# Kernel optimization log

Hardware: AMD Instinct MI355X
Metric: run time of the kernel (lower is better)

Reference implementation:

```python
import jax, jax.numpy as jnp
import numpy as np

N, P, F, E = 4096, 512, 4096, 65536
FN, FE = 32, 32
H, C = 4, 64
D = H * C
HL = 64
LMAX, LFMAX = 256, 16


def _bn(x, g, b):
    m = x.mean(0)
    v = jnp.mean((x - m) ** 2, 0)
    return (x - m) / jnp.sqrt(v + 1e-5) * g + b


def _gat(x, src, dst, eattr, W, We, asrc, adst, aedge, bias):
    # PyG GATConv with edge_dim: self-loops appended with fill_value='mean' edge attrs
    n = x.shape[0]
    cnt = jax.ops.segment_sum(jnp.ones((eattr.shape[0],), eattr.dtype), dst, n)
    sums = jax.ops.segment_sum(eattr, dst, n)
    loop_attr = jnp.where(cnt[:, None] > 0, sums / jnp.maximum(cnt, 1.0)[:, None], 0.0)
    loops = jnp.arange(n, dtype=src.dtype)
    s2 = jnp.concatenate([src, loops])
    d2 = jnp.concatenate([dst, loops])
    ea = jnp.concatenate([eattr, loop_attr], 0)
    h = (x @ W).reshape(n, H, C)
    e = (ea @ We).reshape(-1, H, C)
    logits = jax.nn.leaky_relu((h * asrc).sum(-1)[s2] + (h * adst).sum(-1)[d2] + (e * aedge).sum(-1), 0.2)
    mx = jax.ops.segment_max(logits, d2, n)
    w = jnp.exp(logits - mx[d2])
    alpha = w / jax.ops.segment_sum(w, d2, n)[d2]  # softmax over incoming edges per dst
    out = jax.ops.segment_sum(h[s2] * alpha[:, :, None], d2, n).reshape(n, D) + bias
    return out, s2, d2, alpha


def _lstm(seq, Wih, Whh, bih, bhh):
    # torch single-layer batch_first LSTM; gate order i,f,g,o
    B = seq.shape[0]
    hid = Whh.shape[1]
    def step(carry, xt):
        hp, cp = carry
        z = xt @ Wih.T + hp @ Whh.T + bih + bhh
        i, f, g, o = jnp.split(z, 4, axis=-1)
        c = jax.nn.sigmoid(f) * cp + jax.nn.sigmoid(i) * jnp.tanh(g)
        hh = jax.nn.sigmoid(o) * jnp.tanh(c)
        return (hh, c), hh
    init = (jnp.zeros((B, hid), seq.dtype), jnp.zeros((B, hid), seq.dtype))
    _, ys = jax.lax.scan(step, init, seq.transpose(1, 0, 2))
    return ys.transpose(1, 0, 2)


def _pack(x, mask_f, max_len):
    # scatter node ids into [S, max_len] slots (cumsum positions), then gather x
    mask = mask_f > 0.5
    n, S = mask.shape
    lengths = mask.sum(0)
    pos = jnp.cumsum(mask, 0) - 1
    slot = jnp.where(mask, jnp.arange(S)[None, :] * max_len + pos, S * max_len)
    node_ids = jnp.broadcast_to(jnp.arange(n, dtype=jnp.int32)[:, None], (n, S))
    buf = jnp.zeros(S * max_len + 1, jnp.int32).at[slot.reshape(-1)].set(node_ids.reshape(-1))
    nfs = buf[: S * max_len].reshape(S, max_len)
    valid = jnp.arange(max_len)[None, :] < lengths[:, None]
    seq = jnp.where(valid[:, :, None], x[nfs], 0.0)
    return seq, lengths


def _node_seq(x, mask_f, max_len, Wih, Whh, bih, bhh):
    seq, lengths = _pack(x, mask_f, max_len)
    out = _lstm(seq, Wih, Whh, bih, bhh)
    return out[jnp.arange(seq.shape[0]), lengths - 1]


def _splice(x, src_f, snk_f, emap, alpha, max_len, Wih, Whh, bih, bhh):
    # pair k-th source True with k-th sink True in row-major flatten order (torch masked-select semantics)
    src_m = src_f > 0.5
    snk_m = snk_f > 0.5
    n, S = src_m.shape
    lengths = src_m.sum(0)
    pos = jnp.cumsum(src_m, 0) - 1
    node_ids = jnp.broadcast_to(jnp.arange(n, dtype=jnp.int32)[:, None], (n, S)).reshape(-1)
    srcf = src_m.reshape(-1)
    snkf = snk_m.reshape(-1)
    total = n * S
    rank_snk = jnp.cumsum(snkf) - 1
    snk_by_rank = jnp.zeros(total + 1, jnp.int32).at[jnp.where(snkf, rank_snk, total)].set(node_ids)
    paired = snk_by_rank[jnp.cumsum(srcf) - 1]
    slot = jnp.where(src_m, jnp.arange(S)[None, :] * max_len + pos, S * max_len).reshape(-1)
    sbuf = jnp.zeros(S * max_len + 1, jnp.int32).at[slot].set(node_ids)
    tbuf = jnp.zeros(S * max_len + 1, jnp.int32).at[slot].set(paired)
    sn = sbuf[: S * max_len].reshape(S, max_len)
    tn = tbuf[: S * max_len].reshape(S, max_len)
    att = alpha[emap[sn * n + tn]]  # [S, T, H]
    se = (x[sn].reshape(S, max_len, H, C) * att[..., None]).reshape(S, max_len, D)
    te = (x[tn].reshape(S, max_len, H, C) * att[..., None]).reshape(S, max_len, D)
    emb = jnp.concatenate([se, te], -1)
    valid = jnp.arange(max_len)[None, :] < lengths[:, None]
    emb = jnp.where(valid[:, :, None], emb, 0.0)
    out = _lstm(emb, Wih, Whh, bih, bhh)
    return out[jnp.arange(S), lengths - 1]


def _compat(paths, frags):
    # mismatch-count reformulation of ((path==frag) | ~span_mask).all(0): exact for 0/1 masks
    n = paths.shape[0]
    relevance = (paths.T @ frags) > 0.0
    fb = frags > 0.5
    fs = jnp.argmax(fb, 0)
    fe = n - 1 - jnp.argmax(fb[::-1], 0)
    r = jnp.arange(n)[:, None]
    fmask = ((r >= fs[None, :]) & (r <= fe[None, :])).astype(paths.dtype)
    mism = frags.T @ (1.0 - paths) + (fmask - frags).T @ paths  # [F, P]
    compat = mism.T == 0.0
    pos = (relevance & compat).astype(paths.dtype)
    neg = (relevance & (~compat)).astype(paths.dtype)
    return pos, neg


def reference(x, edge_index, edge_attr, candidate_paths, candidate_paths_source, candidate_paths_sink, path_abundance, fragments, bn_x_g, bn_x_b, bn_e_g, bn_e_b, gat0_W, gat0_We, gat0_asrc, gat0_adst, gat0_aedge, gat0_bias, gat1_W, gat1_We, gat1_asrc, gat1_adst, gat1_aedge, gat1_bias, node_Wih, node_Whh, node_bih, node_bhh, splice_Wih, splice_Whh, splice_bih, splice_bhh, frag_Wih, frag_Whh, frag_bih, frag_bhh, fc1_W, fc1_b, fc2_W, fc2_b):
    xn = _bn(x, bn_x_g, bn_x_b)
    ea = _bn(edge_attr, bn_e_g, bn_e_b)
    src, dst = edge_index[0], edge_index[1]
    h, _, _, _ = _gat(xn, src, dst, ea, gat0_W, gat0_We, gat0_asrc, gat0_adst, gat0_aedge, gat0_bias)
    h = jax.nn.elu(h)
    h, s2, d2, alpha = _gat(h, src, dst, ea, gat1_W, gat1_We, gat1_asrc, gat1_adst, gat1_aedge, gat1_bias)
    h = jax.nn.elu(h)
    n = h.shape[0]
    emap = jnp.zeros(n * n, jnp.int32).at[s2 * n + d2].set(jnp.arange(s2.shape[0], dtype=jnp.int32))
    node_emb = _node_seq(h, candidate_paths, LMAX, node_Wih, node_Whh, node_bih, node_bhh)
    splice_emb = _splice(h, candidate_paths_source, candidate_paths_sink, emap, alpha, LMAX, splice_Wih, splice_Whh, splice_bih, splice_bhh)
    path_emb = jnp.concatenate([node_emb, splice_emb, path_abundance[:, None]], -1)
    frag_emb = _node_seq(h, fragments, LFMAX, frag_Wih, frag_Whh, frag_bih, frag_bhh)
    pos, neg = _compat(candidate_paths, fragments)
    combined = jnp.concatenate([path_emb, pos @ frag_emb, neg @ frag_emb], -1)
    score = jax.nn.relu(combined @ fc1_W.T + fc1_b) @ fc2_W.T + fc2_b
    return jax.nn.sigmoid(score[:, 0])


def setup_inputs():
    rng = np.random.default_rng(0)
    keys = jax.random.split(jax.random.key(0), 40)
    idx = np.arange(N)[:, None]
    ps = rng.integers(0, N - LMAX, P)
    pl = rng.integers(16, LMAX + 1, P)
    cp = ((idx >= ps) & (idx < ps + pl)).astype(np.float32)
    cps = ((idx >= ps) & (idx < ps + pl - 1)).astype(np.float32)
    cpk = ((idx >= ps + 1) & (idx < ps + pl)).astype(np.float32)
    fst = rng.integers(0, N - LFMAX, F)
    fl = rng.integers(2, LFMAX + 1, F)
    fr = ((idx >= fst) & (idx < fst + fl)).astype(np.float32)
    # unique off-diagonal edges; first N-1 are consecutive (n, n+1) so splice lookups hit real edges
    consec = np.arange(N - 1) * (N - 1) + np.arange(N - 1)
    r_rand = rng.choice(N * (N - 1), size=E, replace=False)
    r = np.concatenate([consec, np.setdiff1d(r_rand, consec)])[:E]
    esrc = r // (N - 1)
    rem = r % (N - 1)
    edst = rem + (rem >= esrc)
    edge_index = jnp.asarray(np.stack([esrc, edst]).astype(np.int32))
    g = lambda k, s, sc=0.1: jax.random.normal(keys[k], s, jnp.float32) * sc
    return dict(
        x=g(0, (N, FN), 1.0),
        edge_index=edge_index,
        edge_attr=g(1, (E, FE), 1.0),
        candidate_paths=jnp.asarray(cp),
        candidate_paths_source=jnp.asarray(cps),
        candidate_paths_sink=jnp.asarray(cpk),
        path_abundance=jax.random.uniform(keys[2], (P,)),
        fragments=jnp.asarray(fr),
        bn_x_g=jnp.ones((FN,)), bn_x_b=jnp.zeros((FN,)),
        bn_e_g=jnp.ones((FE,)), bn_e_b=jnp.zeros((FE,)),
        gat0_W=g(3, (FN, D)), gat0_We=g(4, (FE, D)), gat0_asrc=g(5, (H, C)), gat0_adst=g(6, (H, C)), gat0_aedge=g(7, (H, C)), gat0_bias=g(8, (D,)),
        gat1_W=g(9, (D, D)), gat1_We=g(10, (FE, D)), gat1_asrc=g(11, (H, C)), gat1_adst=g(12, (H, C)), gat1_aedge=g(13, (H, C)), gat1_bias=g(14, (D,)),
        node_Wih=g(15, (4 * HL, D)), node_Whh=g(16, (4 * HL, HL)), node_bih=g(17, (4 * HL,)), node_bhh=g(18, (4 * HL,)),
        splice_Wih=g(19, (4 * HL, 2 * D)), splice_Whh=g(20, (4 * HL, HL)), splice_bih=g(21, (4 * HL,)), splice_bhh=g(22, (4 * HL,)),
        frag_Wih=g(23, (4 * HL, D)), frag_Whh=g(24, (4 * HL, HL)), frag_bih=g(25, (4 * HL,)), frag_bhh=g(26, (4 * HL,)),
        fc1_W=g(27, (HL, 4 * HL + 1)), fc1_b=g(28, (HL,)), fc2_W=g(29, (1, HL)), fc2_b=g(30, (1,)),
    )
```

## Files before the change

### kernel.cpp

```cpp
#include <hip/hip_runtime.h>


constexpr int cN = 4096, cP = 512, cE = 65536, cF = 4096, cM = cE + cN;
constexpr int cLMAX = 256;

typedef float f32x4 __attribute__((ext_vector_type(4)));

#define DEV __device__ __forceinline__
DEV float sigf(float x)  { return 1.f / (1.f + __expf(-x)); }
DEV float tanhx(float x) { return 2.f / (1.f + __expf(-2.f * x)) - 1.f; }
DEV float eluf(float x)  { return x > 0.f ? x : (__expf(x) - 1.f); }
DEV float lrelu(float x) { return x > 0.f ? x : 0.2f * x; }

#define LBAR() asm volatile("s_waitcnt lgkmcnt(0)\n\ts_barrier" ::: "memory")

__global__ void init_k(float* bnst, int* deg, int* cursor,
                       int* p_s, int* p_e, int* s_s, int* s_e,
                       int* f_s, int* f_e) {
  int i = blockIdx.x * 256 + threadIdx.x;
  if (i < 128) bnst[i] = 0.f;
  if (i < cN) { deg[i] = 0; cursor[i] = 0; f_s[i] = 0x7fffffff; f_e[i] = -1; }
  if (i < cP) { p_s[i] = 0x7fffffff; p_e[i] = -1; s_s[i] = 0x7fffffff; s_e[i] = -1; }
}

__global__ void bn_stats(const float* __restrict__ x, int rows,
                         float* sums, float* sumsq) {
  int tid = threadIdx.x;
  long total = (long)rows * 32;
  float s = 0.f, q = 0.f;
  for (long i = (long)blockIdx.x * 256 + tid; i < total; i += (long)gridDim.x * 256) {
    float v = x[i]; s += v; q += v * v;
  }
  __shared__ float ls[256], lq[256];
  ls[tid] = s; lq[tid] = q; __syncthreads();
  if (tid < 32) {
    float S = 0.f, Q = 0.f;
    for (int j = tid; j < 256; j += 32) { S += ls[j]; Q += lq[j]; }
    atomicAdd(&sums[tid], S); atomicAdd(&sumsq[tid], Q);
  }
}

__global__ void prep_small(const float* bnst,
    const float* xg, const float* xb, const float* eg, const float* eb,
    const float* We0, const float* ae0, const float* We1, const float* ae1,
    const float* nbih, const float* nbhh, const float* fbih, const float* fbhh,
    const float* sbih, const float* sbhh,
    float* scaleX, float* shiftX, float* scaleE, float* shiftE,
    float* q0, float* q1, float* nb, float* fb, float* sbb) {
  int tid = threadIdx.x;
  if (tid < 32) {
    float m = bnst[tid] / (float)cN;
    float v = bnst[32 + tid] / (float)cN - m * m;
    float sc = xg[tid] * rsqrtf(v + 1e-5f);
    scaleX[tid] = sc; shiftX[tid] = xb[tid] - m * sc;
  } else if (tid < 64) {
    int c = tid - 32;
    float m = bnst[64 + c] / (float)cE;
    float v = bnst[96 + c] / (float)cE - m * m;
    float sc = eg[c] * rsqrtf(v + 1e-5f);
    scaleE[c] = sc; shiftE[c] = eb[c] - m * sc;
  }
  if (tid < 128) {
    int k = tid >> 2, hh = tid & 3;
    float s0 = 0.f, s1 = 0.f;
    for (int c = 0; c < 64; c++) {
      s0 += We0[k * 256 + hh * 64 + c] * ae0[hh * 64 + c];
      s1 += We1[k * 256 + hh * 64 + c] * ae1[hh * 64 + c];
    }
    q0[tid] = s0; q1[tid] = s1;
  }
  nb[tid] = nbih[tid] + nbhh[tid];
  fb[tid] = fbih[tid] + fbhh[tid];
  sbb[tid] = sbih[tid] + sbhh[tid];
}

__global__ void bn_apply(const float* __restrict__ x, const float* __restrict__ e,
                         const float* scX, const float* shX,
                         const float* scE, const float* shE,
                         float* xn, float* ea) {
  long t1 = (long)cN * 32, t2 = t1 + (long)cE * 32;
  for (long i = (long)blockIdx.x * 256 + threadIdx.x; i < t2; i += (long)gridDim.x * 256) {
    if (i < t1) { int c = (int)(i & 31); xn[i] = x[i] * scX[c] + shX[c]; }
    else { long j = i - t1; int c = (int)(j & 31); ea[j] = e[j] * scE[c] + shE[c]; }
  }
}

__global__ void deg_count(const int* __restrict__ ei, int* deg) {
  int m = blockIdx.x * 256 + threadIdx.x;
  if (m < cE) atomicAdd(&deg[ei[cE + m]], 1);
}

__global__ void scan_offsets(const int* __restrict__ deg, int* offs) {
  __shared__ int tsum[256]; __shared__ int tpre[257];
  int tid = threadIdx.x;
  int base = tid * 16, s = 0; int loc[16];
  for (int i = 0; i < 16; i++) { loc[i] = s; s += deg[base + i] + 1; }
  tsum[tid] = s; __syncthreads();
  if (tid == 0) { int r = 0; for (int j = 0; j < 256; j++) { tpre[j] = r; r += tsum[j]; } tpre[256] = r; }
  __syncthreads();
  for (int i = 0; i < 16; i++) offs[base + i] = tpre[tid] + loc[i];
  if (tid == 255) offs[cN] = tpre[256];
}

__global__ void csr_fill(const int* __restrict__ ei, const int* __restrict__ offs,
                         int* cursor, int* eids) {
  int m = blockIdx.x * 256 + threadIdx.x;
  if (m < cE) {
    int d = ei[cE + m];
    int pos = atomicAdd(&cursor[d], 1);
    eids[offs[d] + pos] = m;
  } else if (m < cM) {
    int n = m - cE;
    int pos = atomicAdd(&cursor[n], 1);
    eids[offs[n] + pos] = m;
  }
}

__global__ void loop_attr_k(const float* __restrict__ ea, const int* __restrict__ offs,
                            const int* __restrict__ eids,
                            const float* q0, const float* q1,
                            float* es0, float* es1) {
  int n = blockIdx.x, tid = threadIdx.x;
  __shared__ float la[32];
  int o0 = offs[n], o1 = offs[n + 1];
  if (tid < 32) {
    float s = 0.f; int cnt = 0;
    for (int x = o0; x < o1; x++) {
      int eid = eids[x];
      if (eid < cE) { s += ea[(size_t)eid * 32 + tid]; cnt++; }
    }
    la[tid] = cnt > 0 ? s / (float)cnt : 0.f;
  }
  __syncthreads();
  if (tid < 8) {
    int hh = tid & 3;
    const float* q = (tid < 4) ? q0 : q1;
    float s = 0.f;
    for (int k = 0; k < 32; k++) s += la[k] * q[k * 4 + hh];
    ((tid < 4) ? es0 : es1)[(size_t)(cE + n) * 4 + hh] = s;
  }
}

template <bool NT, bool PERM>
__global__ __launch_bounds__(256) void gemm(const float* __restrict__ A,
                                            const float* __restrict__ B,
                                            const float* __restrict__ bias,
                                            float* __restrict__ C,
                                            int M, int Nc, int K,
                                            int lda, int ldb, int ldc) {
  __shared__ float As[16][65];
  __shared__ float Bs[16][68];
  int nb = Nc / 64;
  int bx = blockIdx.x % nb, by = blockIdx.x / nb;
  int j0 = bx * 64, i0 = by * 64;
  int tid = threadIdx.x, tx = tid % 16, ty = tid / 16;
  float acc[4][4] = {};
  for (int k0 = 0; k0 < K; k0 += 16) {
    for (int l = tid; l < 1024; l += 256) {
      int r = l >> 4, c = l & 15;
      As[c][r] = A[(size_t)(i0 + r) * lda + k0 + c];
    }
    if (NT) {
      for (int l = tid; l < 1024; l += 256) {
        int r = l >> 4, c = l & 15;
        Bs[c][r] = B[(size_t)(j0 + r) * ldb + k0 + c];
      }
    } else {
      for (int l = tid; l < 1024; l += 256) {
        int j = l & 63, c = l >> 6;
        Bs[c][j] = B[(size_t)(k0 + c) * ldb + j0 + j];
      }
    }
    __syncthreads();
#pragma unroll
    for (int kk = 0; kk < 16; kk++) {
      float av[4], bv[4];
#pragma unroll
      for (int u = 0; u < 4; u++) { av[u] = As[kk][ty * 4 + u]; bv[u] = Bs[kk][tx * 4 + u]; }
#pragma unroll
      for (int u = 0; u < 4; u++)
#pragma unroll
        for (int v = 0; v < 4; v++) acc[u][v] = fmaf(av[u], bv[v], acc[u][v]);
    }
    __syncthreads();
  }
#pragma unroll
  for (int u = 0; u < 4; u++)
#pragma unroll
    for (int v = 0; v < 4; v++) {
      int i = i0 + ty * 4 + u, j = j0 + tx * 4 + v;
      float r = acc[u][v] + (bias ? bias[j] : 0.f);
      int jj = PERM ? (((j & 63) << 2) | (j >> 6)) : j;
      C[(size_t)i * ldc + jj] = r;
    }
}

__global__ __launch_bounds__(256) void gemm_g(const float* __restrict__ hf,
                                              const float* __restrict__ sWih,
                                              float* __restrict__ Gp) {
  int bid = blockIdx.x;
  int hh = bid & 3, jt = (bid >> 2) & 3, mt = bid >> 4;
  int i0 = mt * 64, j0 = jt * 64;
  __shared__ float As[16][65];
  __shared__ float Bs[16][68];
  int tid = threadIdx.x, tx = tid & 15, ty = tid >> 4;
  float acc[4][4] = {};
  for (int k0 = 0; k0 < 128; k0 += 16) {
    int second = (k0 >= 64);
    int kb = hh * 64 + (k0 & 63);
    for (int l = tid; l < 1024; l += 256) {
      int r = l >> 4, c = l & 15;
      int row = i0 + r + second;
      As[c][r] = (row < cN) ? hf[(size_t)row * 256 + kb + c] : 0.f;
    }
    for (int l = tid; l < 1024; l += 256) {
      int r = l >> 4, c = l & 15;
      Bs[c][r] = sWih[(size_t)(j0 + r) * 512 + second * 256 + kb + c];
    }
    __syncthreads();
#pragma unroll
    for (int kk = 0; kk < 16; kk++) {
      float av[4], bv[4];
#pragma unroll
      for (int u = 0; u < 4; u++) { av[u] = As[kk][ty * 4 + u]; bv[u] = Bs[kk][tx * 4 + u]; }
#pragma unroll
      for (int u = 0; u < 4; u++)
#pragma unroll
        for (int v = 0; v < 4; v++) acc[u][v] = fmaf(av[u], bv[v], acc[u][v]);
    }
    __syncthreads();
  }
#pragma unroll
  for (int u = 0; u < 4; u++)
#pragma unroll
    for (int v = 0; v < 4; v++) {
      int i = i0 + ty * 4 + u, j = j0 + tx * 4 + v;
      int g = j >> 6, un = j & 63;
      Gp[(size_t)i * 1024 + un * 16 + g * 4 + hh] = acc[u][v];
    }
}

__global__ void node_scores(const float* __restrict__ h, const float* __restrict__ asrc,
                            const float* __restrict__ adst, float* ssrc, float* sdst) {
  int idx = blockIdx.x * 256 + threadIdx.x;
  if (idx >= cN * 4) return;
  int n = idx >> 2, hh = idx & 3;
  float s1 = 0.f, s2 = 0.f;
  const float* hr = h + (size_t)n * 256 + hh * 64;
  const float* a1 = asrc + hh * 64;
  const float* a2 = adst + hh * 64;
  for (int c = 0; c < 64; c++) { float v = hr[c]; s1 += v * a1[c]; s2 += v * a2[c]; }
  ssrc[idx] = s1; sdst[idx] = s2;
}

__global__ void es_edges(const float* __restrict__ ea, const float* __restrict__ q,
                         float* es) {
  int m = blockIdx.x * 256 + threadIdx.x;
  if (m >= cE) return;
  float a0 = 0.f, a1 = 0.f, a2 = 0.f, a3 = 0.f;
  const float4* r4 = (const float4*)(ea + (size_t)m * 32);
#pragma unroll
  for (int k4 = 0; k4 < 8; k4++) {
    float4 v = r4[k4];
    int k = k4 * 4;
    a0 += v.x * q[k * 4] + v.y * q[(k + 1) * 4] + v.z * q[(k + 2) * 4] + v.w * q[(k + 3) * 4];
    a1 += v.x * q[k * 4 + 1] + v.y * q[(k + 1) * 4 + 1] + v.z * q[(k + 2) * 4 + 1] + v.w * q[(k + 3) * 4 + 1];
    a2 += v.x * q[k * 4 + 2] + v.y * q[(k + 1) * 4 + 2] + v.z * q[(k + 2) * 4 + 2] + v.w * q[(k + 3) * 4 + 2];
    a3 += v.x * q[k * 4 + 3] + v.y * q[(k + 1) * 4 + 3] + v.z * q[(k + 2) * 4 + 3] + v.w * q[(k + 3) * 4 + 3];
  }
  float* o = es + (size_t)m * 4;
  o[0] = a0; o[1] = a1; o[2] = a2; o[3] = a3;
}

__global__ __launch_bounds__(256) void gat_agg(
    const float* __restrict__ hfeat, const float* __restrict__ ssrc,
    const float* __restrict__ sdst, const float* __restrict__ es,
    const int* __restrict__ offs, const int* __restrict__ eids,
    const int* __restrict__ ei, const float* __restrict__ bias,
    float* __restrict__ out, float* alpha_out) {
  int n = blockIdx.x, tid = threadIdx.x;
  __shared__ float l_lds[1024 * 4];
  __shared__ int s_lds[1024];
  __shared__ float red[4];
  int o0 = offs[n], o1 = offs[n + 1];
  int deg = o1 - o0; if (deg > 1024) deg = 1024;
  for (int idx = tid; idx < deg * 4; idx += 256) {
    int e = idx >> 2, hh = idx & 3;
    int eid = eids[o0 + e];
    int src = (eid < cE) ? ei[eid] : n;
    if (hh == 0) s_lds[e] = src;
    float lg = ssrc[src * 4 + hh] + sdst[n * 4 + hh] + es[(size_t)eid * 4 + hh];
    l_lds[idx] = lrelu(lg);
  }
  __syncthreads();
  if (tid < 4) {
    float mx = -1e30f;
    for (int e = 0; e < deg; e++) mx = fmaxf(mx, l_lds[e * 4 + tid]);
    float sm = 0.f;
    for (int e = 0; e < deg; e++) {
      float w = __expf(l_lds[e * 4 + tid] - mx);
      l_lds[e * 4 + tid] = w; sm += w;
    }
    red[tid] = 1.f / sm;
  }
  __syncthreads();
  for (int idx = tid; idx < deg * 4; idx += 256) {
    int e = idx >> 2, hh = idx & 3;
    float a = l_lds[idx] * red[hh];
    l_lds[idx] = a;
    if (alpha_out) { int eid = eids[o0 + e]; alpha_out[(size_t)eid * 4 + hh] = a; }
  }
  __syncthreads();
  int c = tid, hh = c >> 6;
  float acc = 0.f;
  for (int e = 0; e < deg; e++)
    acc = fmaf(l_lds[e * 4 + hh], hfeat[(size_t)s_lds[e] * 256 + c], acc);
  acc += bias[c];
  out[(size_t)n * 256 + c] = eluf(acc);
}

__global__ void intervals_k(const float* __restrict__ cp, const float* __restrict__ cps,
                            const float* __restrict__ fr,
                            int* p_s, int* p_e, int* s_s, int* s_e,
                            int* f_s, int* f_e) {
  const long T1 = (long)cN * cP, T2 = 2 * T1, T3 = T2 + (long)cN * cF;
  for (long i = (long)blockIdx.x * 256 + threadIdx.x; i < T3; i += (long)gridDim.x * 256) {
    if (i < T1) {
      if (cp[i] > 0.5f) { int col = (int)(i % cP), row = (int)(i / cP);
        atomicMin(&p_s[col], row); atomicMax(&p_e[col], row); }
    } else if (i < T2) {
      long j = i - T1;
      if (cps[j] > 0.5f) { int col = (int)(j % cP), row = (int)(j / cP);
        atomicMin(&s_s[col], row); atomicMax(&s_e[col], row); }
    } else {
      long j = i - T2;
      if (fr[j] > 0.5f) { int col = (int)(j % cF), row = (int)(j / cF);
        atomicMin(&f_s[col], row); atomicMax(&f_e[col], row); }
    }
  }
}

__global__ void att_prep(const int* __restrict__ s_s, const int* __restrict__ s_e,
                         const int* __restrict__ offs, const int* __restrict__ eids,
                         const int* __restrict__ ei, const float* __restrict__ alpha1,
                         float* att) {
  int idx = blockIdx.x * 256 + threadIdx.x;
  int s = idx / cLMAX, t = idx % cLMAX;
  int ss = s_s[s], len = s_e[s] - ss + 1;
  float4 a4 = make_float4(0.f, 0.f, 0.f, 0.f);
  if (t < len) {
    int a = ss + t, b = a + 1;
    int found = 0;
    for (int x = offs[b]; x < offs[b + 1]; x++) {
      int eid = eids[x];
      int src = (eid < cE) ? ei[eid] : b;
      if (src == a) { found = eid; break; }
    }
    a4 = *(const float4*)&alpha1[(size_t)found * 4];
  }
  *(float4*)&att[(size_t)idx * 4] = a4;
}

__global__ __launch_bounds__(256, 4) void lstm_all(
    const float* __restrict__ Znp, const float* __restrict__ Zfp,
    const float* __restrict__ Gp, const float* __restrict__ att,
    const float* __restrict__ WhhN, const float* __restrict__ WhhS,
    const float* __restrict__ WhhF, const float* __restrict__ sbias,
    const int* __restrict__ p_s, const int* __restrict__ p_e,
    const int* __restrict__ s_s, const int* __restrict__ s_e,
    const int* __restrict__ f_s, const int* __restrict__ f_e,
    float* node_emb, float* spl_emb, float* frag_emb) {
  int b = blockIdx.x;
  int tid = threadIdx.x;
  int w = tid >> 6, lane = tid & 63;
  int g = lane & 3, ul = lane >> 2;
  int unit = w * 16 + ul;
  int role, sid;
  if (b < cP) { role = 0; sid = b; }
  else if (b < 2 * cP) { role = 1; sid = b - cP; }
  else { role = 2; sid = b - 2 * cP; }

  const float* Whh = (role == 0) ? WhhN : (role == 1 ? WhhS : WhhF);
  const float* wrow = Whh + (size_t)(g * 64 + unit) * 64;
  float wv[64];
#pragma unroll
  for (int k = 0; k < 16; k++) {
    f32x4 v = *(const f32x4*)(wrow + 4 * k);
    wv[4 * k] = v.x; wv[4 * k + 1] = v.y; wv[4 * k + 2] = v.z; wv[4 * k + 3] = v.w;
  }
#pragma unroll
  for (int k = 0; k < 64; k++) asm volatile("" : "+v"(wv[k]));

  int start, len;
  if (role == 0) { start = p_s[sid]; len = p_e[sid] - start + 1; }
  else if (role == 1) { start = s_s[sid]; len = s_e[sid] - start + 1; }
  else { start = f_s[sid]; len = f_e[sid] - start + 1; }

  float sb = (role == 1) ? sbias[g * 64 + unit] : 0.f;

  const float* Zb = (role == 0) ? Znp : Zfp;
  __shared__ float hbuf[2][64];
  if (tid < 64) hbuf[0][tid] = 0.f;
  float cc = 0.f, h = 0.f;

  float zc = 0.f; f32x4 gc = {0.f, 0.f, 0.f, 0.f}, atc = gc;
  if (role == 1) {
    gc = *(const f32x4*)(Gp + (size_t)start * 1024 + tid * 4);
    atc = *(const f32x4*)(att + (size_t)sid * cLMAX * 4);
  } else {
    zc = Zb[(size_t)start * 256 + tid];
  }
  LBAR();

  for (int t = 0; t < len; t++) {
    int rb = t & 1;
    float zin = (role == 1)
        ? sb + atc.x * gc.x + atc.y * gc.y + atc.z * gc.z + atc.w * gc.w
        : zc;

    float znx = zc; f32x4 gnx = gc, atn = atc;
    if (t + 1 < len) {
      if (role == 1) {
        gnx = *(const f32x4*)(Gp + (size_t)(start + t + 1) * 1024 + tid * 4);
        atn = *(const f32x4*)(att + (size_t)(sid * cLMAX + t + 1) * 4);
      } else {
        znx = Zb[(size_t)(start + t + 1) * 256 + tid];
      }
    }

    float za = zin, zb2 = 0.f;
#pragma unroll
    for (int kc = 0; kc < 8; kc++) {
      f32x4 hv = *(const f32x4*)&hbuf[rb][4 * kc];
      za = fmaf(hv.x, wv[4 * kc], za);     za = fmaf(hv.y, wv[4 * kc + 1], za);
      za = fmaf(hv.z, wv[4 * kc + 2], za); za = fmaf(hv.w, wv[4 * kc + 3], za);
    }
#pragma unroll
    for (int kc = 8; kc < 16; kc++) {
      f32x4 hv = *(const f32x4*)&hbuf[rb][4 * kc];
      zb2 = fmaf(hv.x, wv[4 * kc], zb2);     zb2 = fmaf(hv.y, wv[4 * kc + 1], zb2);
      zb2 = fmaf(hv.z, wv[4 * kc + 2], zb2); zb2 = fmaf(hv.w, wv[4 * kc + 3], zb2);
    }
    float z = za + zb2;

    int base = lane & ~3;
    float zi = __shfl(z, base, 64);
    float zf = __shfl(z, base + 1, 64);
    float zg = __shfl(z, base + 2, 64);
    float zo = __shfl(z, base + 3, 64);

    float gi = sigf(zi), gf = sigf(zf), gg = tanhx(zg), go = sigf(zo);
    cc = gf * cc + gi * gg;
    h = go * tanhx(cc);

    if (g == 0) hbuf[rb ^ 1][unit] = h;
    LBAR();

    zc = znx; gc = gnx; atc = atn;
  }

  float* dst = (role == 0) ? node_emb : (role == 1 ? spl_emb : frag_emb);
  if (g == 0) dst[(size_t)sid * 64 + unit] = h;
}

__global__ __launch_bounds__(256) void score_final(
    const float* __restrict__ femb, const int* __restrict__ p_s,
    const int* __restrict__ p_e, const int* __restrict__ f_s,
    const int* __restrict__ f_e, const float* __restrict__ nemb,
    const float* __restrict__ semb, const float* __restrict__ abund,
    const float* __restrict__ fc1W, const float* __restrict__ fc1b,
    const float* __restrict__ fc2W, const float* __restrict__ fc2b,
    float* out) {
  int p = blockIdx.x, tid = threadIdx.x;
  __shared__ float cmb[257];
  __shared__ float accp[256], accn[256], r1[64];
  int ps = p_s[p], pe = p_e[p];
  int d = tid & 63, g = tid >> 6;
  float ap = 0.f, an = 0.f;
  for (int f = g; f < cF; f += 4) {
    int fs = f_s[f], fe = f_e[f];
    if (fs <= pe && fe >= ps) {
      float v = femb[(size_t)f * 64 + d];
      if (fs >= ps && fe <= pe) ap += v;
      else an += v;
    }
  }
  accp[tid] = ap; accn[tid] = an; __syncthreads();
  if (tid < 64) {
    cmb[tid] = nemb[(size_t)p * 64 + tid];
    cmb[64 + tid] = semb[(size_t)p * 64 + tid];
    cmb[129 + tid] = accp[tid] + accp[tid + 64] + accp[tid + 128] + accp[tid + 192];
    cmb[193 + tid] = accn[tid] + accn[tid + 64] + accn[tid + 128] + accn[tid + 192];
    if (tid == 0) cmb[128] = abund[p];
  }
  __syncthreads();
  if (tid < 64) {
    float s = fc1b[tid];
    for (int k = 0; k < 257; k++) s = fmaf(cmb[k], fc1W[tid * 257 + k], s);
    r1[tid] = s > 0.f ? s : 0.f;
  }
  __syncthreads();
  if (tid == 0) {
    float s = fc2b[0];
    for (int j = 0; j < 64; j++) s = fmaf(r1[j], fc2W[j], s);
    out[p] = 1.f / (1.f + __expf(-s));
  }
}

extern "C" void kernel_launch(void* const* d_in, const int* in_sizes, int n_in,
                              void* d_out, int out_size, void* d_ws, size_t ws_size,
                              hipStream_t stream) {
  (void)in_sizes; (void)n_in; (void)out_size; (void)ws_size;
  const float* x     = (const float*)d_in[0];
  const int*   ei    = (const int*)  d_in[1];
  const float* eattr = (const float*)d_in[2];
  const float* cp    = (const float*)d_in[3];
  const float* cps   = (const float*)d_in[4];
  const float* abund = (const float*)d_in[6];
  const float* frg   = (const float*)d_in[7];
  const float* bnxg  = (const float*)d_in[8];
  const float* bnxb  = (const float*)d_in[9];
  const float* bneg  = (const float*)d_in[10];
  const float* bneb  = (const float*)d_in[11];
  const float* g0W   = (const float*)d_in[12];
  const float* g0We  = (const float*)d_in[13];
  const float* g0as  = (const float*)d_in[14];
  const float* g0ad  = (const float*)d_in[15];
  const float* g0ae  = (const float*)d_in[16];
  const float* g0b   = (const float*)d_in[17];
  const float* g1W   = (const float*)d_in[18];
  const float* g1We  = (const float*)d_in[19];
  const float* g1as  = (const float*)d_in[20];
  const float* g1ad  = (const float*)d_in[21];
  const float* g1ae  = (const float*)d_in[22];
  const float* g1b   = (const float*)d_in[23];
  const float* nWih  = (const float*)d_in[24];
  const float* nWhh  = (const float*)d_in[25];
  const float* nbih  = (const float*)d_in[26];
  const float* nbhh  = (const float*)d_in[27];
  const float* sWih  = (const float*)d_in[28];
  const float* sWhh  = (const float*)d_in[29];
  const float* sbih  = (const float*)d_in[30];
  const float* sbhh  = (const float*)d_in[31];
  const float* fWih  = (const float*)d_in[32];
  const float* fWhh  = (const float*)d_in[33];
  const float* fbih  = (const float*)d_in[34];
  const float* fbhh  = (const float*)d_in[35];
  const float* fc1W  = (const float*)d_in[36];
  const float* fc1b  = (const float*)d_in[37];
  const float* fc2W  = (const float*)d_in[38];
  const float* fc2b  = (const float*)d_in[39];
  float* out = (float*)d_out;

  char* base = (char*)d_ws;
  size_t used = 0;
  auto alloc = [&](size_t nbytes) -> char* {
    char* p = base + used;
    used += (nbytes + 255) & ~(size_t)255;
    return p;
  };
  float* bnst   = (float*)alloc(128 * 4);
  float* scaleX = (float*)alloc(32 * 4);
  float* shiftX = (float*)alloc(32 * 4);
  float* scaleE = (float*)alloc(32 * 4);
  float* shiftE = (float*)alloc(32 * 4);
  float* q0     = (float*)alloc(128 * 4);
  float* q1     = (float*)alloc(128 * 4);
  float* nb     = (float*)alloc(256 * 4);
  float* fb     = (float*)alloc(256 * 4);
  float* sbb    = (float*)alloc(256 * 4);
  float* xn     = (float*)alloc((size_t)cN * 32 * 4);
  float* eab    = (float*)alloc((size_t)cE * 32 * 4);
  float* h0     = (float*)alloc((size_t)cN * 256 * 4);
  float* h0e    = (float*)alloc((size_t)cN * 256 * 4);
  float* h1     = (float*)alloc((size_t)cN * 256 * 4);
  float* hf     = (float*)alloc((size_t)cN * 256 * 4);
  float* ssrc0  = (float*)alloc((size_t)cN * 4 * 4);
  float* sdst0  = (float*)alloc((size_t)cN * 4 * 4);
  float* ssrc1  = (float*)alloc((size_t)cN * 4 * 4);
  float* sdst1  = (float*)alloc((size_t)cN * 4 * 4);
  float* es0    = (float*)alloc((size_t)cM * 4 * 4);
  float* es1    = (float*)alloc((size_t)cM * 4 * 4);
  float* alpha1 = (float*)alloc((size_t)cM * 4 * 4);
  float* Znp    = (float*)alloc((size_t)cN * 256 * 4);
  float* Zfp    = (float*)alloc((size_t)cN * 256 * 4);
  float* Gp     = (float*)alloc((size_t)cN * 1024 * 4);
  float* attb   = (float*)alloc((size_t)cP * cLMAX * 4 * 4);
  float* nemb   = (float*)alloc((size_t)cP * 64 * 4);
  float* semb   = (float*)alloc((size_t)cP * 64 * 4);
  float* femb   = (float*)alloc((size_t)cF * 64 * 4);
  int* deg    = (int*)alloc(cN * 4);
  int* cursor = (int*)alloc(cN * 4);
  int* offs   = (int*)alloc((cN + 1) * 4);
  int* eidsA  = (int*)alloc(cM * 4);
  int* p_s = (int*)alloc(cP * 4); int* p_e = (int*)alloc(cP * 4);
  int* s_s = (int*)alloc(cP * 4); int* s_e = (int*)alloc(cP * 4);
  int* f_s = (int*)alloc(cF * 4); int* f_e = (int*)alloc(cF * 4);

  init_k<<<16, 256, 0, stream>>>(bnst, deg, cursor, p_s, p_e, s_s, s_e, f_s, f_e);
  bn_stats<<<64, 256, 0, stream>>>(x, cN, bnst, bnst + 32);
  bn_stats<<<256, 256, 0, stream>>>(eattr, cE, bnst + 64, bnst + 96);
  prep_small<<<1, 256, 0, stream>>>(bnst, bnxg, bnxb, bneg, bneb,
      g0We, g0ae, g1We, g1ae, nbih, nbhh, fbih, fbhh, sbih, sbhh,
      scaleX, shiftX, scaleE, shiftE, q0, q1, nb, fb, sbb);
  bn_apply<<<2048, 256, 0, stream>>>(x, eattr, scaleX, shiftX, scaleE, shiftE, xn, eab);

  deg_count<<<cE / 256, 256, 0, stream>>>(ei, deg);
  scan_offsets<<<1, 256, 0, stream>>>(deg, offs);
  csr_fill<<<(cM + 255) / 256, 256, 0, stream>>>(ei, offs, cursor, eidsA);
  loop_attr_k<<<cN, 64, 0, stream>>>(eab, offs, eidsA, q0, q1, es0, es1);

  intervals_k<<<4096, 256, 0, stream>>>(cp, cps, frg, p_s, p_e, s_s, s_e, f_s, f_e);

  gemm<false, false><<<(4096 / 64) * (256 / 64), 256, 0, stream>>>(xn, g0W, nullptr, h0, 4096, 256, 32, 32, 256, 256);
  node_scores<<<64, 256, 0, stream>>>(h0, g0as, g0ad, ssrc0, sdst0);
  es_edges<<<256, 256, 0, stream>>>(eab, q0, es0);
  gat_agg<<<cN, 256, 0, stream>>>(h0, ssrc0, sdst0, es0, offs, eidsA, ei, g0b, h0e, nullptr);
  gemm<false, false><<<(4096 / 64) * (256 / 64), 256, 0, stream>>>(h0e, g1W, nullptr, h1, 4096, 256, 256, 256, 256, 256);
  node_scores<<<64, 256, 0, stream>>>(h1, g1as, g1ad, ssrc1, sdst1);
  es_edges<<<256, 256, 0, stream>>>(eab, q1, es1);
  gat_agg<<<cN, 256, 0, stream>>>(h1, ssrc1, sdst1, es1, offs, eidsA, ei, g1b, hf, alpha1);

  gemm<true, true><<<(4096 / 64) * (256 / 64), 256, 0, stream>>>(hf, nWih, nb, Znp, 4096, 256, 256, 256, 256, 256);
  gemm<true, true><<<(4096 / 64) * (256 / 64), 256, 0, stream>>>(hf, fWih, fb, Zfp, 4096, 256, 256, 256, 256, 256);
  gemm_g<<<64 * 4 * 4, 256, 0, stream>>>(hf, sWih, Gp);
  att_prep<<<(cP * cLMAX) / 256, 256, 0, stream>>>(s_s, s_e, offs, eidsA, ei, alpha1, attb);

  lstm_all<<<2 * cP + cF, 256, 0, stream>>>(Znp, Zfp, Gp, attb, nWhh, sWhh, fWhh, sbb,
      p_s, p_e, s_s, s_e, f_s, f_e, nemb, semb, femb);

  score_final<<<cP, 256, 0, stream>>>(femb, p_s, p_e, f_s, f_e, nemb, semb, abund,
      fc1W, fc1b, fc2W, fc2b, out);
}
```

Baseline: 810.2 us.

## Split LSTM recurrent dot product across two thread halves with shared-memory reduction

The fused LSTM kernel now launches 512 threads per block instead of 256. Each half of the block holds 32 of the 64 recurrent weights per row and computes a partial dot product with the hidden state. The upper half writes its partials to shared memory, and the lower half adds them and applies the gate nonlinearities. This shortens the serial FMA chain per timestep and cuts per-thread weight registers, at the cost of an extra barrier and a shared-memory round-trip every step.

```diff
diff --git a/kernel.cpp b/kernel.cpp
--- a/kernel.cpp
+++ b/kernel.cpp
@@ -361,7 +361,7 @@
   *(float4*)&att[(size_t)idx * 4] = a4;
 }
 
-__global__ __launch_bounds__(256, 4) void lstm_all(
+__global__ __launch_bounds__(512) void lstm_all(
     const float* __restrict__ Znp, const float* __restrict__ Zfp,
     const float* __restrict__ Gp, const float* __restrict__ att,
     const float* __restrict__ WhhN, const float* __restrict__ WhhS,
@@ -373,23 +373,21 @@
   int b = blockIdx.x;
   int tid = threadIdx.x;
   int w = tid >> 6, lane = tid & 63;
+  int kh = w >> 2;
+  int wq = w & 3;
   int g = lane & 3, ul = lane >> 2;
-  int unit = w * 16 + ul;
+  int unit = wq * 16 + ul;
   int role, sid;
   if (b < cP) { role = 0; sid = b; }
   else if (b < 2 * cP) { role = 1; sid = b - cP; }
   else { role = 2; sid = b - 2 * cP; }
 
   const float* Whh = (role == 0) ? WhhN : (role == 1 ? WhhS : WhhF);
-  const float* wrow = Whh + (size_t)(g * 64 + unit) * 64;
-  float wv[64];
-#pragma unroll
-  for (int k = 0; k < 16; k++) {
-    f32x4 v = *(const f32x4*)(wrow + 4 * k);
-    wv[4 * k] = v.x; wv[4 * k + 1] = v.y; wv[4 * k + 2] = v.z; wv[4 * k + 3] = v.w;
-  }
-#pragma unroll
-  for (int k = 0; k < 64; k++) asm volatile("" : "+v"(wv[k]));
+  const float* wrow = Whh + (size_t)(g * 64 + unit) * 64 + kh * 32;
+  f32x4 w0 = *(const f32x4*)(wrow + 0),  w1 = *(const f32x4*)(wrow + 4);
+  f32x4 w2 = *(const f32x4*)(wrow + 8),  w3 = *(const f32x4*)(wrow + 12);
+  f32x4 w4 = *(const f32x4*)(wrow + 16), w5 = *(const f32x4*)(wrow + 20);
+  f32x4 w6 = *(const f32x4*)(wrow + 24), w7 = *(const f32x4*)(wrow + 28);
 
   int start, len;
   if (role == 0) { start = p_s[sid]; len = p_e[sid] - start + 1; }
@@ -400,67 +398,93 @@
 
   const float* Zb = (role == 0) ? Znp : Zfp;
   __shared__ float hbuf[2][64];
+  __shared__ float zpart[256];
   if (tid < 64) hbuf[0][tid] = 0.f;
   float cc = 0.f, h = 0.f;
 
   float zc = 0.f; f32x4 gc = {0.f, 0.f, 0.f, 0.f}, atc = gc;
-  if (role == 1) {
-    gc = *(const f32x4*)(Gp + (size_t)start * 1024 + tid * 4);
-    atc = *(const f32x4*)(att + (size_t)sid * cLMAX * 4);
-  } else {
-    zc = Zb[(size_t)start * 256 + tid];
+  if (kh == 0) {
+    if (role == 1) {
+      gc = *(const f32x4*)(Gp + (size_t)start * 1024 + (unit * 16 + g * 4));
+      atc = *(const f32x4*)(att + (size_t)sid * cLMAX * 4);
+    } else {
+      zc = Zb[(size_t)start * 256 + unit * 4 + g];
+    }
   }
   LBAR();
 
   for (int t = 0; t < len; t++) {
     int rb = t & 1;
-    float zin = (role == 1)
-        ? sb + atc.x * gc.x + atc.y * gc.y + atc.z * gc.z + atc.w * gc.w
-        : zc;
+    float za = 0.f;
+    if (kh == 0) {
+      za = (role == 1)
+          ? sb + atc.x * gc.x + atc.y * gc.y + atc.z * gc.z + atc.w * gc.w
+          : zc;
+    }
 
     float znx = zc; f32x4 gnx = gc, atn = atc;
-    if (t + 1 < len) {
+    if (kh == 0 && t + 1 < len) {
       if (role == 1) {
-        gnx = *(const f32x4*)(Gp + (size_t)(start + t + 1) * 1024 + tid * 4);
+        gnx = *(const f32x4*)(Gp + (size_t)(start + t + 1) * 1024 + (unit * 16 + g * 4));
         atn = *(const f32x4*)(att + (size_t)(sid * cLMAX + t + 1) * 4);
       } else {
-        znx = Zb[(size_t)(start + t + 1) * 256 + tid];
+        znx = Zb[(size_t)(start + t + 1) * 256 + unit * 4 + g];
       }
     }
 
-    float za = zin, zb2 = 0.f;
-#pragma unroll
-    for (int kc = 0; kc < 8; kc++) {
-      f32x4 hv = *(const f32x4*)&hbuf[rb][4 * kc];
-      za = fmaf(hv.x, wv[4 * kc], za);     za = fmaf(hv.y, wv[4 * kc + 1], za);
-      za = fmaf(hv.z, wv[4 * kc + 2], za); za = fmaf(hv.w, wv[4 * kc + 3], za);
-    }
-#pragma unroll
-    for (int kc = 8; kc < 16; kc++) {
-      f32x4 hv = *(const f32x4*)&hbuf[rb][4 * kc];
-      zb2 = fmaf(hv.x, wv[4 * kc], zb2);     zb2 = fmaf(hv.y, wv[4 * kc + 1], zb2);
-      zb2 = fmaf(hv.z, wv[4 * kc + 2], zb2); zb2 = fmaf(hv.w, wv[4 * kc + 3], zb2);
-    }
-    float z = za + zb2;
-
-    int base = lane & ~3;
-    float zi = __shfl(z, base, 64);
-    float zf = __shfl(z, base + 1, 64);
-    float zg = __shfl(z, base + 2, 64);
-    float zo = __shfl(z, base + 3, 64);
-
-    float gi = sigf(zi), gf = sigf(zf), gg = tanhx(zg), go = sigf(zo);
-    cc = gf * cc + gi * gg;
-    h = go * tanhx(cc);
-
-    if (g == 0) hbuf[rb ^ 1][unit] = h;
+    const float* hrow = &hbuf[rb][kh * 32];
+    float zb2 = 0.f;
+    {
+      f32x4 hv;
+      hv = *(const f32x4*)(hrow + 0);
+      za = fmaf(hv.x, w0.x, za); za = fmaf(hv.y, w0.y, za);
+      za = fmaf(hv.z, w0.z, za); za = fmaf(hv.w, w0.w, za);
+      hv = *(const f32x4*)(hrow + 4);
+      zb2 = fmaf(hv.x, w1.x, zb2); zb2 = fmaf(hv.y, w1.y, zb2);
+      zb2 = fmaf(hv.z, w1.z, zb2); zb2 = fmaf(hv.w, w1.w, zb2);
+      hv = *(const f32x4*)(hrow + 8);
+      za = fmaf(hv.x, w2.x, za); za = fmaf(hv.y, w2.y, za);
+      za = fmaf(hv.z, w2.z, za); za = fmaf(hv.w, w2.w, za);
+      hv = *(const f32x4*)(hrow + 12);
+      zb2 = fmaf(hv.x, w3.x, zb2); zb2 = fmaf(hv.y, w3.y, zb2);
+      zb2 = fmaf(hv.z, w3.z, zb2); zb2 = fmaf(hv.w, w3.w, zb2);
+      hv = *(const f32x4*)(hrow + 16);
+      za = fmaf(hv.x, w4.x, za); za = fmaf(hv.y, w4.y, za);
+      za = fmaf(hv.z, w4.z, za); za = fmaf(hv.w, w4.w, za);
+      hv = *(const f32x4*)(hrow + 20);
+      zb2 = fmaf(hv.x, w5.x, zb2); zb2 = fmaf(hv.y, w5.y, zb2);
+      zb2 = fmaf(hv.z, w5.z, zb2); zb2 = fmaf(hv.w, w5.w, zb2);
+      hv = *(const f32x4*)(hrow + 24);
+      za = fmaf(hv.x, w6.x, za); za = fmaf(hv.y, w6.y, za);
+      za = fmaf(hv.z, w6.z, za); za = fmaf(hv.w, w6.w, za);
+      hv = *(const f32x4*)(hrow + 28);
+      zb2 = fmaf(hv.x, w7.x, zb2); zb2 = fmaf(hv.y, w7.y, zb2);
+      zb2 = fmaf(hv.z, w7.z, zb2); zb2 = fmaf(hv.w, w7.w, zb2);
+    }
+    float zp = za + zb2;
+
+    if (kh == 1) zpart[wq * 64 + lane] = zp;
     LBAR();
 
+    if (kh == 0) {
+      float z = zp + zpart[wq * 64 + lane];
+      int base = lane & ~3;
+      float zi = __shfl(z, base, 64);
+      float zf = __shfl(z, base + 1, 64);
+      float zg = __shfl(z, base + 2, 64);
+      float zo = __shfl(z, base + 3, 64);
+      float gi = sigf(zi), gf = sigf(zf), gg = tanhx(zg), go = sigf(zo);
+      cc = gf * cc + gi * gg;
+      h = go * tanhx(cc);
+      if (g == 0) hbuf[rb ^ 1][unit] = h;
+    }
+    LBAR();
+
     zc = znx; gc = gnx; atc = atn;
   }
 
   float* dst = (role == 0) ? node_emb : (role == 1 ? spl_emb : frag_emb);
-  if (g == 0) dst[(size_t)sid * 64 + unit] = h;
+  if (kh == 0 && g == 0) dst[(size_t)sid * 64 + unit] = h;
 }
 
 __global__ __launch_bounds__(256) void score_final(
@@ -626,7 +650,7 @@
   gemm_g<<<64 * 4 * 4, 256, 0, stream>>>(hf, sWih, Gp);
   att_prep<<<(cP * cLMAX) / 256, 256, 0, stream>>>(s_s, s_e, offs, eidsA, ei, alpha1, attb);
 
-  lstm_all<<<2 * cP + cF, 256, 0, stream>>>(Znp, Zfp, Gp, attb, nWhh, sWhh, fWhh, sbb,
+  lstm_all<<<2 * cP + cF, 512, 0, stream>>>(Znp, Zfp, Gp, attb, nWhh, sWhh, fWhh, sbb,
       p_s, p_e, s_s, s_e, f_s, f_e, nemb, semb, femb);
 
   score_final<<<cP, 256, 0, stream>>>(femb, p_s, p_e, f_s, f_e, nemb, semb, abund,
```

New measurement: 836.2 us. 1.03x slower.

## Batch four LSTM sequences per block with shared-memory recurrent weights

Applied to the files above, without the earlier changes.

Restructures the LSTM kernel so each 512-thread block processes four sequences at once. The recurrent weight matrix is staged in LDS instead of per-thread registers, and the K dimension is split across two thread halves with an LDS reduction. Producer GEMM output layouts change so each gate row is read contiguously. This amortizes weight loads and shortens the grid, but every step now needs three barriers, and the block runs for the longest of its four sequences, wasting steps on the shorter ones.

```diff
diff --git a/kernel.cpp b/kernel.cpp
--- a/kernel.cpp
+++ b/kernel.cpp
@@ -141,7 +141,7 @@
   }
 }
 
-template <bool NT, bool PERM>
+template <bool NT>
 __global__ __launch_bounds__(256) void gemm(const float* __restrict__ A,
                                             const float* __restrict__ B,
                                             const float* __restrict__ bias,
@@ -190,8 +190,7 @@
     for (int v = 0; v < 4; v++) {
       int i = i0 + ty * 4 + u, j = j0 + tx * 4 + v;
       float r = acc[u][v] + (bias ? bias[j] : 0.f);
-      int jj = PERM ? (((j & 63) << 2) | (j >> 6)) : j;
-      C[(size_t)i * ldc + jj] = r;
+      C[(size_t)i * ldc + j] = r;
     }
 }
 
@@ -236,7 +235,7 @@
     for (int v = 0; v < 4; v++) {
       int i = i0 + ty * 4 + u, j = j0 + tx * 4 + v;
       int g = j >> 6, un = j & 63;
-      Gp[(size_t)i * 1024 + un * 16 + g * 4 + hh] = acc[u][v];
+      Gp[(size_t)i * 1024 + g * 256 + un * 4 + hh] = acc[u][v];
     }
 }
 
@@ -361,7 +360,7 @@
   *(float4*)&att[(size_t)idx * 4] = a4;
 }
 
-__global__ __launch_bounds__(256, 4) void lstm_all(
+__global__ __launch_bounds__(512) void lstm_all(
     const float* __restrict__ Znp, const float* __restrict__ Zfp,
     const float* __restrict__ Gp, const float* __restrict__ att,
     const float* __restrict__ WhhN, const float* __restrict__ WhhS,
@@ -370,97 +369,142 @@
     const int* __restrict__ s_s, const int* __restrict__ s_e,
     const int* __restrict__ f_s, const int* __restrict__ f_e,
     float* node_emb, float* spl_emb, float* frag_emb) {
-  int b = blockIdx.x;
-  int tid = threadIdx.x;
-  int w = tid >> 6, lane = tid & 63;
-  int g = lane & 3, ul = lane >> 2;
-  int unit = w * 16 + ul;
-  int role, sid;
-  if (b < cP) { role = 0; sid = b; }
-  else if (b < 2 * cP) { role = 1; sid = b - cP; }
-  else { role = 2; sid = b - 2 * cP; }
+  int b = blockIdx.x, tid = threadIdx.x;
+  int role, sbase;
+  if (b < 128) { role = 0; sbase = b * 4; }
+  else if (b < 256) { role = 1; sbase = (b - 128) * 4; }
+  else { role = 2; sbase = (b - 256) * 4; }
 
   const float* Whh = (role == 0) ? WhhN : (role == 1 ? WhhS : WhhF);
-  const float* wrow = Whh + (size_t)(g * 64 + unit) * 64;
-  float wv[64];
-#pragma unroll
-  for (int k = 0; k < 16; k++) {
-    f32x4 v = *(const f32x4*)(wrow + 4 * k);
-    wv[4 * k] = v.x; wv[4 * k + 1] = v.y; wv[4 * k + 2] = v.z; wv[4 * k + 3] = v.w;
-  }
-#pragma unroll
-  for (int k = 0; k < 64; k++) asm volatile("" : "+v"(wv[k]));
-
-  int start, len;
-  if (role == 0) { start = p_s[sid]; len = p_e[sid] - start + 1; }
-  else if (role == 1) { start = s_s[sid]; len = s_e[sid] - start + 1; }
-  else { start = f_s[sid]; len = f_e[sid] - start + 1; }
-
-  float sb = (role == 1) ? sbias[g * 64 + unit] : 0.f;
-
+  const int* Ss = (role == 0) ? p_s : (role == 1 ? s_s : f_s);
+  const int* Se = (role == 0) ? p_e : (role == 1 ? s_e : f_e);
+
+  __shared__ float Wl[256 * 66];
+  __shared__ float zbuf[256 * 4];
+  __shared__ float hbuf[2][64 * 4];
+
+#pragma unroll
+  for (int p = 0; p < 8; p++) {
+    int flat = (p * 512 + tid) * 4;
+    int row = flat >> 6, k = flat & 63;
+    f32x4 v = *(const f32x4*)(Whh + flat);
+    *(f32x4*)&Wl[row * 66 + k] = v;
+  }
+  if (tid < 256) hbuf[0][tid] = 0.f;
+
+  int r = tid & 255, kh = tid >> 8;
+  int u = tid & 63, sP = (tid >> 6) & 3;
+
+  int st0 = Ss[sbase], st1 = Ss[sbase + 1], st2 = Ss[sbase + 2], st3 = Ss[sbase + 3];
+  int l0 = Se[sbase] - st0 + 1, l1 = Se[sbase + 1] - st1 + 1;
+  int l2 = Se[sbase + 2] - st2 + 1, l3 = Se[sbase + 3] - st3 + 1;
+  int maxlen = max(max(l0, l1), max(l2, l3));
+  int stP = 0, lnP = 0;
+  if (kh == 0) { stP = Ss[sbase + sP]; lnP = Se[sbase + sP] - stP + 1; }
+  (void)stP;
+
+  float sb = (role == 1 && kh == 0) ? sbias[r] : 0.f;
   const float* Zb = (role == 0) ? Znp : Zfp;
-  __shared__ float hbuf[2][64];
-  if (tid < 64) hbuf[0][tid] = 0.f;
+
+  float zp0 = 0, zp1 = 0, zp2 = 0, zp3 = 0;
+  f32x4 gq0 = {0,0,0,0}, gq1 = gq0, gq2 = gq0, gq3 = gq0;
+  f32x4 at0 = gq0, at1 = gq0, at2 = gq0, at3 = gq0;
+  int goff = ((r >> 6) << 8) | ((r & 63) << 2);
+  if (kh == 0) {
+    if (role == 1) {
+      gq0 = *(const f32x4*)(Gp + (size_t)st0 * 1024 + goff);
+      gq1 = *(const f32x4*)(Gp + (size_t)st1 * 1024 + goff);
+      gq2 = *(const f32x4*)(Gp + (size_t)st2 * 1024 + goff);
+      gq3 = *(const f32x4*)(Gp + (size_t)st3 * 1024 + goff);
+      at0 = *(const f32x4*)(att + (size_t)(sbase + 0) * cLMAX * 4);
+      at1 = *(const f32x4*)(att + (size_t)(sbase + 1) * cLMAX * 4);
+      at2 = *(const f32x4*)(att + (size_t)(sbase + 2) * cLMAX * 4);
+      at3 = *(const f32x4*)(att + (size_t)(sbase + 3) * cLMAX * 4);
+    } else {
+      zp0 = Zb[(size_t)st0 * 256 + r];
+      zp1 = Zb[(size_t)st1 * 256 + r];
+      zp2 = Zb[(size_t)st2 * 256 + r];
+      zp3 = Zb[(size_t)st3 * 256 + r];
+    }
+  }
   float cc = 0.f, h = 0.f;
-
-  float zc = 0.f; f32x4 gc = {0.f, 0.f, 0.f, 0.f}, atc = gc;
-  if (role == 1) {
-    gc = *(const f32x4*)(Gp + (size_t)start * 1024 + tid * 4);
-    atc = *(const f32x4*)(att + (size_t)sid * cLMAX * 4);
-  } else {
-    zc = Zb[(size_t)start * 256 + tid];
-  }
-  LBAR();
-
-  for (int t = 0; t < len; t++) {
-    int rb = t & 1;
-    float zin = (role == 1)
-        ? sb + atc.x * gc.x + atc.y * gc.y + atc.z * gc.z + atc.w * gc.w
-        : zc;
-
-    float znx = zc; f32x4 gnx = gc, atn = atc;
-    if (t + 1 < len) {
+  __syncthreads();
+
+  const float* wb = &Wl[r * 66 + kh * 32];
+
+  for (int t = 0; t < maxlen; t++) {
+    int cur = t & 1;
+    float a0 = 0, a1 = 0, a2 = 0, a3 = 0;
+    if (kh == 0) {
       if (role == 1) {
-        gnx = *(const f32x4*)(Gp + (size_t)(start + t + 1) * 1024 + tid * 4);
-        atn = *(const f32x4*)(att + (size_t)(sid * cLMAX + t + 1) * 4);
+        a0 = sb + at0.x * gq0.x + at0.y * gq0.y + at0.z * gq0.z + at0.w * gq0.w;
+        a1 = sb + at1.x * gq1.x + at1.y * gq1.y + at1.z * gq1.z + at1.w * gq1.w;
+        a2 = sb + at2.x * gq2.x + at2.y * gq2.y + at2.z * gq2.z + at2.w * gq2.w;
+        a3 = sb + at3.x * gq3.x + at3.y * gq3.y + at3.z * gq3.z + at3.w * gq3.w;
+      } else { a0 = zp0; a1 = zp1; a2 = zp2; a3 = zp3; }
+    }
+
+    if (kh == 0 && t + 1 < maxlen) {
+      if (role == 1) {
+        if (t + 1 < l0) { gq0 = *(const f32x4*)(Gp + (size_t)(st0 + t + 1) * 1024 + goff);
+                          at0 = *(const f32x4*)(att + ((size_t)(sbase + 0) * cLMAX + t + 1) * 4); }
+        if (t + 1 < l1) { gq1 = *(const f32x4*)(Gp + (size_t)(st1 + t + 1) * 1024 + goff);
+                          at1 = *(const f32x4*)(att + ((size_t)(sbase + 1) * cLMAX + t + 1) * 4); }
+        if (t + 1 < l2) { gq2 = *(const f32x4*)(Gp + (size_t)(st2 + t + 1) * 1024 + goff);
+                          at2 = *(const f32x4*)(att + ((size_t)(sbase + 2) * cLMAX + t + 1) * 4); }
+        if (t + 1 < l3) { gq3 = *(const f32x4*)(Gp + (size_t)(st3 + t + 1) * 1024 + goff);
+                          at3 = *(const f32x4*)(att + ((size_t)(sbase + 3) * cLMAX + t + 1) * 4); }
       } else {
-        znx = Zb[(size_t)(start + t + 1) * 256 + tid];
+        if (t + 1 < l0) zp0 = Zb[(size_t)(st0 + t + 1) * 256 + r];
+        if (t + 1 < l1) zp1 = Zb[(size_t)(st1 + t + 1) * 256 + r];
+        if (t + 1 < l2) zp2 = Zb[(size_t)(st2 + t + 1) * 256 + r];
+        if (t + 1 < l3) zp3 = Zb[(size_t)(st3 + t + 1) * 256 + r];
       }
     }
 
-    float za = zin, zb2 = 0.f;
-#pragma unroll
-    for (int kc = 0; kc < 8; kc++) {
-      f32x4 hv = *(const f32x4*)&hbuf[rb][4 * kc];
-      za = fmaf(hv.x, wv[4 * kc], za);     za = fmaf(hv.y, wv[4 * kc + 1], za);
-      za = fmaf(hv.z, wv[4 * kc + 2], za); za = fmaf(hv.w, wv[4 * kc + 3], za);
-    }
-#pragma unroll
-    for (int kc = 8; kc < 16; kc++) {
-      f32x4 hv = *(const f32x4*)&hbuf[rb][4 * kc];
-      zb2 = fmaf(hv.x, wv[4 * kc], zb2);     zb2 = fmaf(hv.y, wv[4 * kc + 1], zb2);
-      zb2 = fmaf(hv.z, wv[4 * kc + 2], zb2); zb2 = fmaf(hv.w, wv[4 * kc + 3], zb2);
-    }
-    float z = za + zb2;
-
-    int base = lane & ~3;
-    float zi = __shfl(z, base, 64);
-    float zf = __shfl(z, base + 1, 64);
-    float zg = __shfl(z, base + 2, 64);
-    float zo = __shfl(z, base + 3, 64);
-
-    float gi = sigf(zi), gf = sigf(zf), gg = tanhx(zg), go = sigf(zo);
-    cc = gf * cc + gi * gg;
-    h = go * tanhx(cc);
-
-    if (g == 0) hbuf[rb ^ 1][unit] = h;
+    const float* hc = &hbuf[cur][kh * 128];
+#pragma unroll
+    for (int q = 0; q < 8; q++) {
+      f32x4 wq = *(const f32x4*)(wb + q * 4);
+      f32x4 h0 = *(const f32x4*)(hc + q * 16);
+      f32x4 h1 = *(const f32x4*)(hc + q * 16 + 4);
+      f32x4 h2 = *(const f32x4*)(hc + q * 16 + 8);
+      f32x4 h3 = *(const f32x4*)(hc + q * 16 + 12);
+      a0 = fmaf(wq.x, h0.x, a0); a1 = fmaf(wq.x, h0.y, a1);
+      a2 = fmaf(wq.x, h0.z, a2); a3 = fmaf(wq.x, h0.w, a3);
+      a0 = fmaf(wq.y, h1.x, a0); a1 = fmaf(wq.y, h1.y, a1);
+      a2 = fmaf(wq.y, h1.z, a2); a3 = fmaf(wq.y, h1.w, a3);
+      a0 = fmaf(wq.z, h2.x, a0); a1 = fmaf(wq.z, h2.y, a1);
+      a2 = fmaf(wq.z, h2.z, a2); a3 = fmaf(wq.z, h2.w, a3);
+      a0 = fmaf(wq.w, h3.x, a0); a1 = fmaf(wq.w, h3.y, a1);
+      a2 = fmaf(wq.w, h3.z, a2); a3 = fmaf(wq.w, h3.w, a3);
+    }
+
+    if (kh == 1) { f32x4 v = {a0, a1, a2, a3}; *(f32x4*)&zbuf[r * 4] = v; }
     LBAR();
-
-    zc = znx; gc = gnx; atc = atn;
-  }
-
-  float* dst = (role == 0) ? node_emb : (role == 1 ? spl_emb : frag_emb);
-  if (g == 0) dst[(size_t)sid * 64 + unit] = h;
+    if (kh == 0) {
+      f32x4 zp = *(const f32x4*)&zbuf[r * 4];
+      f32x4 v = {a0 + zp.x, a1 + zp.y, a2 + zp.z, a3 + zp.w};
+      *(f32x4*)&zbuf[r * 4] = v;
+    }
+    LBAR();
+    if (kh == 0 && t < lnP) {
+      float zi = zbuf[(u)*4 + sP];
+      float zf = zbuf[(64 + u) * 4 + sP];
+      float zg = zbuf[(128 + u) * 4 + sP];
+      float zo = zbuf[(192 + u) * 4 + sP];
+      float gi = sigf(zi), gf = sigf(zf), gg = tanhx(zg), go = sigf(zo);
+      cc = gf * cc + gi * gg;
+      h = go * tanhx(cc);
+      hbuf[cur ^ 1][u * 4 + sP] = h;
+    }
+    LBAR();
+  }
+
+  if (kh == 0) {
+    float* dst = (role == 0) ? node_emb : (role == 1 ? spl_emb : frag_emb);
+    dst[(size_t)(sbase + sP) * 64 + u] = h;
+  }
 }
 
 __global__ __launch_bounds__(256) void score_final(
@@ -612,21 +656,21 @@
 
   intervals_k<<<4096, 256, 0, stream>>>(cp, cps, frg, p_s, p_e, s_s, s_e, f_s, f_e);
 
-  gemm<false, false><<<(4096 / 64) * (256 / 64), 256, 0, stream>>>(xn, g0W, nullptr, h0, 4096, 256, 32, 32, 256, 256);
+  gemm<false><<<(4096 / 64) * (256 / 64), 256, 0, stream>>>(xn, g0W, nullptr, h0, 4096, 256, 32, 32, 256, 256);
   node_scores<<<64, 256, 0, stream>>>(h0, g0as, g0ad, ssrc0, sdst0);
   es_edges<<<256, 256, 0, stream>>>(eab, q0, es0);
   gat_agg<<<cN, 256, 0, stream>>>(h0, ssrc0, sdst0, es0, offs, eidsA, ei, g0b, h0e, nullptr);
-  gemm<false, false><<<(4096 / 64) * (256 / 64), 256, 0, stream>>>(h0e, g1W, nullptr, h1, 4096, 256, 256, 256, 256, 256);
+  gemm<false><<<(4096 / 64) * (256 / 64), 256, 0, stream>>>(h0e, g1W, nullptr, h1, 4096, 256, 256, 256, 256, 256);
   node_scores<<<64, 256, 0, stream>>>(h1, g1as, g1ad, ssrc1, sdst1);
   es_edges<<<256, 256, 0, stream>>>(eab, q1, es1);
   gat_agg<<<cN, 256, 0, stream>>>(h1, ssrc1, sdst1, es1, offs, eidsA, ei, g1b, hf, alpha1);
 
-  gemm<true, true><<<(4096 / 64) * (256 / 64), 256, 0, stream>>>(hf, nWih, nb, Znp, 4096, 256, 256, 256, 256, 256);
-  gemm<true, true><<<(4096 / 64) * (256 / 64), 256, 0, stream>>>(hf, fWih, fb, Zfp, 4096, 256, 256, 256, 256, 256);
+  gemm<true><<<(4096 / 64) * (256 / 64), 256, 0, stream>>>(hf, nWih, nb, Znp, 4096, 256, 256, 256, 256, 256);
+  gemm<true><<<(4096 / 64) * (256 / 64), 256, 0, stream>>>(hf, fWih, fb, Zfp, 4096, 256, 256, 256, 256, 256);
   gemm_g<<<64 * 4 * 4, 256, 0, stream>>>(hf, sWih, Gp);
   att_prep<<<(cP * cLMAX) / 256, 256, 0, stream>>>(s_s, s_e, offs, eidsA, ei, alpha1, attb);
 
-  lstm_all<<<2 * cP + cF, 256, 0, stream>>>(Znp, Zfp, Gp, attb, nWhh, sWhh, fWhh, sbb,
+  lstm_all<<<1280, 512, 0, stream>>>(Znp, Zfp, Gp, attb, nWhh, sWhh, fWhh, sbb,
       p_s, p_e, s_s, s_e, f_s, f_e, nemb, semb, femb);
 
   score_final<<<cP, 256, 0, stream>>>(femb, p_s, p_e, f_s, f_e, nemb, semb, abund,
```

New measurement: 1.306 ms. +61.2%, slower.
